# Performance work log

Hardware: AMD Instinct MI355X
Metric: run time of the kernel (lower is better)

The kernel has to match this reference:

```python
import jax, jax.numpy as jnp
import numpy as np

N_NODES = 100000
N_EDGES = 3200000
OUT_CH = 128
X_DIM = 128


def setup_inputs() -> dict:
    key = jax.random.key(0)
    k1, k2, k3, k4 = jax.random.split(key, 4)
    x = jax.random.normal(k1, (N_NODES, X_DIM), dtype=jnp.float32)
    edge_index = jax.random.randint(k2, (2, N_EDGES), 0, N_NODES, dtype=jnp.int64)
    # torch nn.Linear(num_nodes, out_channels): weight [out, N], bias [out]
    W_weight = jax.random.normal(k3, (OUT_CH, N_NODES), dtype=jnp.float32) * (1.0 / np.sqrt(N_NODES))
    W_bias = jax.random.normal(k4, (OUT_CH,), dtype=jnp.float32) * 0.01
    return {"x": x, "edge_index": edge_index, "W_weight": W_weight, "W_bias": W_bias}


def reference(x, edge_index, W_weight, W_bias):
    """LINK forward: logits = A @ W.T + b, A = sparse COO adjacency from edge_index.

    A[r, c] = 1 for each edge (r, c), so row r of the output is
    sum_{c in neighbors(r)} W.T[c] + b  -> gather + segment_sum (SpMM).
    """
    N = x.shape[0]
    row, col = edge_index[0], edge_index[1]
    Wt = W_weight.T  # [N, out]
    gathered = Wt[col]  # [E, out] irregular gather
    logits = jax.ops.segment_sum(gathered, row, num_segments=N) + W_bias  # [N, out]
    return logits
```

## Files before the change

### kernel.cpp

```cpp
#include <hip/hip_runtime.h>


#define NCHUNK 512
#define STRIDE 6656
#define MAXB 1600
#define CAP 3072

__global__ __launch_bounds__(256) void absmax_kernel(const float* __restrict__ W,
                                                     int n4,
                                                     unsigned int* __restrict__ amax) {
    int i = blockIdx.x * blockDim.x + threadIdx.x;
    int stride = gridDim.x * blockDim.x;
    float m = 0.f;
    const float4* W4 = (const float4*)W;
    for (; i < n4; i += stride) {
        float4 v = W4[i];
        m = fmaxf(m, fmaxf(fmaxf(fabsf(v.x), fabsf(v.y)),
                           fmaxf(fabsf(v.z), fabsf(v.w))));
    }
    for (int off = 32; off > 0; off >>= 1) m = fmaxf(m, __shfl_xor(m, off));
    if ((threadIdx.x & 63) == 0) atomicMax(amax, __float_as_uint(m));
}

__global__ __launch_bounds__(256) void quant_kernel(const float* __restrict__ W,
                                                    unsigned char* __restrict__ Wt8,
                                                    const unsigned int* __restrict__ amax,
                                                    int N) {
    __shared__ float tile[128][33];
    int cx = threadIdx.x;
    int oy = threadIdx.y;
    int c = blockIdx.x * 32 + cx;
    for (int k = 0; k < 16; ++k) {
        int o = oy * 16 + k;
        tile[o][cx] = (c < N) ? W[(size_t)o * N + c] : 0.f;
    }
    __syncthreads();
    float M = __uint_as_float(*amax);
    float si = (M > 0.f) ? 127.f / M : 0.f;
    if (c < N) {
        unsigned int w[4];
#pragma unroll
        for (int d = 0; d < 4; ++d) {
            unsigned int acc = 0;
#pragma unroll
            for (int b = 0; b < 4; ++b) {
                int o = oy * 16 + d * 4 + b;
                int qi = __float2int_rn(tile[o][cx] * si) + 128;
                acc |= ((unsigned int)(qi & 0xff)) << (8 * b);
            }
            w[d] = acc;
        }
        *(uint4*)(Wt8 + (size_t)c * 128 + oy * 16) =
            make_uint4(w[0], w[1], w[2], w[3]);
    }
}

__global__ __launch_bounds__(512) void sortchunk(const int* __restrict__ row,
                                                 const int* __restrict__ col,
                                                 int E, int chr_, int nbuck,
                                                 unsigned* __restrict__ packed,
                                                 unsigned* __restrict__ runinfo) {
    __shared__ int lh[MAXB];
    __shared__ int ls[MAXB];
    __shared__ int part[512];
    int c = blockIdx.x, tid = threadIdx.x;
    int s = c * chr_;
    int e = min(E, s + chr_);
    int cnt = e - s;
    for (int k = tid; k < MAXB; k += 512) lh[k] = 0;
    __syncthreads();
    int rst[13], cst[13];
#pragma unroll
    for (int j = 0; j < 13; ++j) {
        int i = j * 512 + tid;
        rst[j] = -1;
        cst[j] = 0;
        if (i < cnt) {
            rst[j] = row[s + i];
            cst[j] = col[s + i];
            atomicAdd(&lh[rst[j] >> 6], 1);
        }
    }
    __syncthreads();
    int b4 = tid * 4;
    int v0 = (b4 + 0 < nbuck) ? lh[b4 + 0] : 0;
    int v1 = (b4 + 1 < nbuck) ? lh[b4 + 1] : 0;
    int v2 = (b4 + 2 < nbuck) ? lh[b4 + 2] : 0;
    int v3 = (b4 + 3 < nbuck) ? lh[b4 + 3] : 0;
    int mysum = v0 + v1 + v2 + v3;
    part[tid] = mysum;
    __syncthreads();
    for (int off = 1; off < 512; off <<= 1) {
        int t = (tid >= off) ? part[tid - off] : 0;
        __syncthreads();
        part[tid] += t;
        __syncthreads();
    }
    {
        int excl = part[tid] - mysum;
        if (b4 + 0 < nbuck) ls[b4 + 0] = excl;
        if (b4 + 1 < nbuck) ls[b4 + 1] = excl + v0;
        if (b4 + 2 < nbuck) ls[b4 + 2] = excl + v0 + v1;
        if (b4 + 3 < nbuck) ls[b4 + 3] = excl + v0 + v1 + v2;
    }
    __syncthreads();
    for (int k = tid; k < nbuck; k += 512)
        runinfo[(size_t)c * nbuck + k] =
            ((unsigned)ls[k] << 13) | (unsigned)lh[k];
    __syncthreads();
    unsigned* dst = packed + (size_t)c * STRIDE;
#pragma unroll
    for (int j = 0; j < 13; ++j) {
        if (rst[j] >= 0) {
            int p = atomicAdd(&ls[rst[j] >> 6], 1);
            dst[p] = ((unsigned)(rst[j] & 63) << 17) | (unsigned)cst[j];
        }
    }
}

__global__ __launch_bounds__(256) void merge_runs(const unsigned* __restrict__ packed,
                                                  const unsigned* __restrict__ runinfo,
                                                  int nbuck,
                                                  unsigned* __restrict__ colsorted,
                                                  int* __restrict__ cntk) {
    __shared__ int part[256];
    int k = blockIdx.x, tid = threadIdx.x;
    unsigned ri0 = runinfo[(size_t)tid * nbuck + k];
    unsigned ri1 = runinfo[(size_t)(tid + 256) * nbuck + k];
    int len0 = ri0 & 0x1FFFu, loc0 = ri0 >> 13;
    int len1 = ri1 & 0x1FFFu, loc1 = ri1 >> 13;
    int mysum = len0 + len1;
    part[tid] = mysum;
    __syncthreads();
    for (int off = 1; off < 256; off <<= 1) {
        int t = (tid >= off) ? part[tid - off] : 0;
        __syncthreads();
        part[tid] += t;
        __syncthreads();
    }
    int excl = part[tid] - mysum;
    if (tid == 255) cntk[k] = min(part[255], CAP);
    unsigned* dstp = colsorted + (size_t)k * CAP;
    const unsigned* s0 = packed + (size_t)tid * STRIDE + loc0;
    for (int j = 0; j < len0; ++j)
        if (excl + j < CAP) dstp[excl + j] = s0[j];
    int d1 = excl + len0;
    const unsigned* s1 = packed + (size_t)(tid + 256) * STRIDE + loc1;
    for (int j = 0; j < len1; ++j)
        if (d1 + j < CAP) dstp[d1 + j] = s1[j];
}

__global__ __launch_bounds__(256) void spmm_fused(
    const unsigned* __restrict__ colsorted, const int* __restrict__ cntk,
    const unsigned char* __restrict__ Wt8, const float* __restrict__ bias,
    const unsigned int* __restrict__ amax, float* __restrict__ out, int N) {
    __shared__ unsigned g2[CAP];
    __shared__ int rhist[64];
    __shared__ int rs[65];
    __shared__ int cur[64];
    __shared__ int sc2[64];
    int k = blockIdx.x, tid = threadIdx.x;
    int cnt = cntk[k];
    const unsigned* src = colsorted + (size_t)k * CAP;
    if (tid < 64) rhist[tid] = 0;
    __syncthreads();
    for (int i = tid; i < cnt; i += 256) atomicAdd(&rhist[src[i] >> 17], 1);
    __syncthreads();
    if (tid < 64) sc2[tid] = rhist[tid];
    __syncthreads();
    for (int off = 1; off < 64; off <<= 1) {
        int t = 0;
        if (tid < 64 && tid >= off) t = sc2[tid - off];
        __syncthreads();
        if (tid < 64) sc2[tid] += t;
        __syncthreads();
    }
    if (tid < 64) {
        rs[tid] = sc2[tid] - rhist[tid];
        cur[tid] = rs[tid];
        if (tid == 63) rs[64] = sc2[63];
    }
    __syncthreads();
    for (int i = tid; i < cnt; i += 256) {
        unsigned v = src[i];
        int p = atomicAdd(&cur[v >> 17], 1);
        g2[p] = (v & 0x1FFFFu) << 7;
    }
    __syncthreads();

    float sg = __uint_as_float(*amax) / 127.f;
    int wave = tid >> 6, lane = tid & 63;
    int h = lane >> 5;
    int lane4 = (lane & 31) * 4;

    for (int r = wave; r < 64; r += 4) {
        int gr = k * 64 + r;
        if (gr >= N) break;
        int js = rs[r], je = rs[r + 1];
        int m = je - js;
        int T = m >> 1;
        unsigned accA = 0, accB = 0;
        int idx = js + h;
        int t = 0;
        for (; t + 4 <= T; t += 4) {
            unsigned e0 = g2[idx + 0];
            unsigned e1 = g2[idx + 2];
            unsigned e2 = g2[idx + 4];
            unsigned e3 = g2[idx + 6];
            idx += 8;
            uint32_t u0 = *(const uint32_t*)(Wt8 + e0 + lane4);
            uint32_t u1 = *(const uint32_t*)(Wt8 + e1 + lane4);
            uint32_t u2 = *(const uint32_t*)(Wt8 + e2 + lane4);
            uint32_t u3 = *(const uint32_t*)(Wt8 + e3 + lane4);
            accA += (u0 & 0x00FF00FFu);
            accB += ((u0 >> 8) & 0x00FF00FFu);
            accA += (u1 & 0x00FF00FFu);
            accB += ((u1 >> 8) & 0x00FF00FFu);
            accA += (u2 & 0x00FF00FFu);
            accB += ((u2 >> 8) & 0x00FF00FFu);
            accA += (u3 & 0x00FF00FFu);
            accB += ((u3 >> 8) & 0x00FF00FFu);
        }
        for (; t < T; ++t) {
            unsigned e0 = g2[idx];
            idx += 2;
            uint32_t u0 = *(const uint32_t*)(Wt8 + e0 + lane4);
            accA += (u0 & 0x00FF00FFu);
            accB += ((u0 >> 8) & 0x00FF00FFu);
        }
        if ((m & 1) && h == 0) {
            unsigned e0 = g2[je - 1];
            uint32_t u0 = *(const uint32_t*)(Wt8 + e0 + lane4);
            accA += (u0 & 0x00FF00FFu);
            accB += ((u0 >> 8) & 0x00FF00FFu);
        }
        accA += __shfl_xor(accA, 32);
        accB += __shfl_xor(accB, 32);
        if (h == 0) {
            float fm = -128.f * (float)m;
            float4 b4 = *(const float4*)(bias + lane4);
            float4 res;
            res.x = fmaf(sg, (float)(accA & 0xffffu) + fm, b4.x);
            res.y = fmaf(sg, (float)(accB & 0xffffu) + fm, b4.y);
            res.z = fmaf(sg, (float)(accA >> 16) + fm, b4.z);
            res.w = fmaf(sg, (float)(accB >> 16) + fm, b4.w);
            *(float4*)(out + (size_t)gr * 128 + lane4) = res;
        }
    }
}

extern "C" void kernel_launch(void* const* d_in, const int* in_sizes, int n_in,
                              void* d_out, int out_size, void* d_ws,
                              size_t ws_size, hipStream_t stream) {
    const int* edge = (const int*)d_in[1];
    const float* W = (const float*)d_in[2];
    const float* bias = (const float*)d_in[3];
    float* out = (float*)d_out;

    const int N = in_sizes[0] / 128;
    const int E = in_sizes[1] / 2;
    const int* row = edge;
    const int* col = edge + E;

    const int nbuck = (N + 63) / 64;
    const int chr_ = (E + NCHUNK - 1) / NCHUNK;

    auto align16 = [](size_t v) { return (v + 15) & ~(size_t)15; };
    char* ws = (char*)d_ws;
    size_t off = 0;
    unsigned char* Wt8 = (unsigned char*)(ws + off);
    off = align16(off + (size_t)N * 128);
    unsigned* packed = (unsigned*)(ws + off);
    off = align16(off + (size_t)NCHUNK * STRIDE * sizeof(unsigned));
    unsigned* runinfo = (unsigned*)(ws + off);
    off = align16(off + (size_t)NCHUNK * nbuck * sizeof(unsigned));
    unsigned* colsorted = (unsigned*)(ws + off);
    off = align16(off + (size_t)nbuck * CAP * sizeof(unsigned));
    int* cntk = (int*)(ws + off);
    off = align16(off + (size_t)nbuck * sizeof(int));
    unsigned int* amax = (unsigned int*)(ws + off);
    off = align16(off + 16);

    hipMemsetAsync(amax, 0, sizeof(unsigned int), stream);

    absmax_kernel<<<1024, 256, 0, stream>>>(W, (128 * N) / 4, amax);
    {
        dim3 block(32, 8);
        dim3 grid((N + 31) / 32);
        quant_kernel<<<grid, block, 0, stream>>>(W, Wt8, amax, N);
    }
    sortchunk<<<NCHUNK, 512, 0, stream>>>(row, col, E, chr_, nbuck, packed,
                                          runinfo);
    merge_runs<<<nbuck, 256, 0, stream>>>(packed, runinfo, nbuck, colsorted,
                                          cntk);
    spmm_fused<<<nbuck, 256, 0, stream>>>(colsorted, cntk, Wt8, bias, amax, out,
                                          N);
}
```

Baseline: 214.9 us.

## Stage sorted runs in LDS and move per-row counting sort into merge kernel

sortchunk now scatters into a shared-memory buffer and then writes the packed array to global memory with coalesced stores, instead of scattering directly to global. The within-bucket row sort moves from spmm_fused into the merge kernel (now gather_group), which stages runs in LDS and writes fully row-sorted, pre-shifted entries plus row starts. This makes global writes coalesced and shortens the spmm kernel's prologue. The trade-off is more LDS use per block (about 26KB in sortchunk and 24KB in gather_group), which may lower occupancy, and an extra global array of row starts.

```diff
diff --git a/kernel.cpp b/kernel.cpp
--- a/kernel.cpp
+++ b/kernel.cpp
@@ -60,6 +60,7 @@
                                                  int E, int chr_, int nbuck,
                                                  unsigned* __restrict__ packed,
                                                  unsigned* __restrict__ runinfo) {
+    __shared__ unsigned g2[STRIDE];
     __shared__ int lh[MAXB];
     __shared__ int ls[MAXB];
     __shared__ int part[512];
@@ -108,22 +109,32 @@
         runinfo[(size_t)c * nbuck + k] =
             ((unsigned)ls[k] << 13) | (unsigned)lh[k];
     __syncthreads();
-    unsigned* dst = packed + (size_t)c * STRIDE;
 #pragma unroll
     for (int j = 0; j < 13; ++j) {
         if (rst[j] >= 0) {
             int p = atomicAdd(&ls[rst[j] >> 6], 1);
-            dst[p] = ((unsigned)(rst[j] & 63) << 17) | (unsigned)cst[j];
-        }
-    }
-}
-
-__global__ __launch_bounds__(256) void merge_runs(const unsigned* __restrict__ packed,
-                                                  const unsigned* __restrict__ runinfo,
-                                                  int nbuck,
-                                                  unsigned* __restrict__ colsorted,
-                                                  int* __restrict__ cntk) {
+            g2[p] = ((unsigned)(rst[j] & 63) << 17) | (unsigned)cst[j];
+        }
+    }
+    __syncthreads();
+    unsigned* dst = packed + (size_t)c * STRIDE;
+#pragma unroll
+    for (int j = 0; j < 13; ++j) {
+        int i = j * 512 + tid;
+        if (i < cnt) dst[i] = g2[i];
+    }
+}
+
+__global__ __launch_bounds__(256) void gather_group(
+    const unsigned* __restrict__ packed, const unsigned* __restrict__ runinfo,
+    int nbuck, unsigned* __restrict__ colsorted, int* __restrict__ rowstartg) {
+    __shared__ unsigned stage[CAP];
+    __shared__ unsigned g3[CAP];
     __shared__ int part[256];
+    __shared__ int rhist[64];
+    __shared__ int rs[65];
+    __shared__ int cur[64];
+    __shared__ int sc2[64];
     int k = blockIdx.x, tid = threadIdx.x;
     unsigned ri0 = runinfo[(size_t)tid * nbuck + k];
     unsigned ri1 = runinfo[(size_t)(tid + 256) * nbuck + k];
@@ -139,32 +150,20 @@
         __syncthreads();
     }
     int excl = part[tid] - mysum;
-    if (tid == 255) cntk[k] = min(part[255], CAP);
-    unsigned* dstp = colsorted + (size_t)k * CAP;
-    const unsigned* s0 = packed + (size_t)tid * STRIDE + loc0;
-    for (int j = 0; j < len0; ++j)
-        if (excl + j < CAP) dstp[excl + j] = s0[j];
-    int d1 = excl + len0;
-    const unsigned* s1 = packed + (size_t)(tid + 256) * STRIDE + loc1;
-    for (int j = 0; j < len1; ++j)
-        if (d1 + j < CAP) dstp[d1 + j] = s1[j];
-}
-
-__global__ __launch_bounds__(256) void spmm_fused(
-    const unsigned* __restrict__ colsorted, const int* __restrict__ cntk,
-    const unsigned char* __restrict__ Wt8, const float* __restrict__ bias,
-    const unsigned int* __restrict__ amax, float* __restrict__ out, int N) {
-    __shared__ unsigned g2[CAP];
-    __shared__ int rhist[64];
-    __shared__ int rs[65];
-    __shared__ int cur[64];
-    __shared__ int sc2[64];
-    int k = blockIdx.x, tid = threadIdx.x;
-    int cnt = cntk[k];
-    const unsigned* src = colsorted + (size_t)k * CAP;
+    int tot = part[255];
+    int cnt = min(tot, CAP);
+    {
+        const unsigned* s0 = packed + (size_t)tid * STRIDE + loc0;
+        for (int j = 0; j < len0; ++j)
+            if (excl + j < CAP) stage[excl + j] = s0[j];
+        int d1 = excl + len0;
+        const unsigned* s1 = packed + (size_t)(tid + 256) * STRIDE + loc1;
+        for (int j = 0; j < len1; ++j)
+            if (d1 + j < CAP) stage[d1 + j] = s1[j];
+    }
     if (tid < 64) rhist[tid] = 0;
     __syncthreads();
-    for (int i = tid; i < cnt; i += 256) atomicAdd(&rhist[src[i] >> 17], 1);
+    for (int i = tid; i < cnt; i += 256) atomicAdd(&rhist[stage[i] >> 17], 1);
     __syncthreads();
     if (tid < 64) sc2[tid] = rhist[tid];
     __syncthreads();
@@ -182,16 +181,35 @@
     }
     __syncthreads();
     for (int i = tid; i < cnt; i += 256) {
-        unsigned v = src[i];
+        unsigned v = stage[i];
         int p = atomicAdd(&cur[v >> 17], 1);
-        g2[p] = (v & 0x1FFFFu) << 7;
-    }
+        g3[p] = (v & 0x1FFFFu) << 7;
+    }
+    __syncthreads();
+    unsigned* dstp = colsorted + (size_t)k * CAP;
+    for (int i = tid; i < cnt; i += 256) dstp[i] = g3[i];
+    if (tid < 65) rowstartg[(size_t)k * 65 + tid] = rs[tid];
+}
+
+__global__ __launch_bounds__(256) void spmm_fused(
+    const unsigned* __restrict__ colsorted, const int* __restrict__ rowstartg,
+    const unsigned char* __restrict__ Wt8, const float* __restrict__ bias,
+    const unsigned int* __restrict__ amax, float* __restrict__ out, int N) {
+    __shared__ unsigned g2[CAP];
+    __shared__ int rs[65];
+    int k = blockIdx.x, tid = threadIdx.x;
+    if (tid < 65) rs[tid] = rowstartg[(size_t)k * 65 + tid];
+    __syncthreads();
+    int cnt = rs[64];
+    const unsigned* src = colsorted + (size_t)k * CAP;
+    for (int i = tid; i < cnt; i += 256) g2[i] = src[i];
     __syncthreads();
 
     float sg = __uint_as_float(*amax) / 127.f;
     int wave = tid >> 6, lane = tid & 63;
     int h = lane >> 5;
     int lane4 = (lane & 31) * 4;
+    float4 b4 = *(const float4*)(bias + lane4);
 
     for (int r = wave; r < 64; r += 4) {
         int gr = k * 64 + r;
@@ -238,7 +256,6 @@
         accB += __shfl_xor(accB, 32);
         if (h == 0) {
             float fm = -128.f * (float)m;
-            float4 b4 = *(const float4*)(bias + lane4);
             float4 res;
             res.x = fmaf(sg, (float)(accA & 0xffffu) + fm, b4.x);
             res.y = fmaf(sg, (float)(accB & 0xffffu) + fm, b4.y);
@@ -276,8 +293,8 @@
     off = align16(off + (size_t)NCHUNK * nbuck * sizeof(unsigned));
     unsigned* colsorted = (unsigned*)(ws + off);
     off = align16(off + (size_t)nbuck * CAP * sizeof(unsigned));
-    int* cntk = (int*)(ws + off);
-    off = align16(off + (size_t)nbuck * sizeof(int));
+    int* rowstartg = (int*)(ws + off);
+    off = align16(off + (size_t)nbuck * 65 * sizeof(int));
     unsigned int* amax = (unsigned int*)(ws + off);
     off = align16(off + 16);
 
@@ -291,8 +308,8 @@
     }
     sortchunk<<<NCHUNK, 512, 0, stream>>>(row, col, E, chr_, nbuck, packed,
                                           runinfo);
-    merge_runs<<<nbuck, 256, 0, stream>>>(packed, runinfo, nbuck, colsorted,
-                                          cntk);
-    spmm_fused<<<nbuck, 256, 0, stream>>>(colsorted, cntk, Wt8, bias, amax, out,
-                                          N);
-}
+    gather_group<<<nbuck, 256, 0, stream>>>(packed, runinfo, nbuck, colsorted,
+                                            rowstartg);
+    spmm_fused<<<nbuck, 256, 0, stream>>>(colsorted, rowstartg, Wt8, bias, amax,
+                                          out, N);
+}
```

Measured after the change: 186.2 us. 1.15x faster.
